# Performance work log

Measured on AMD Instinct MI355X. Metric: run time of the kernel, lower is better.

Reference implementation:

```python
import jax, jax.numpy as jnp
import numpy as np

OUT_FEATURES = 8192
IN_FEATURES = 4096  # d
CODEBOOK_SIZE = 16  # 2**bits, bits=4
BATCH = 32


def setup_inputs() -> dict:
    key = jax.random.key(0)
    k_x, k_idx, k_cb, k_r, k_b = jax.random.split(key, 5)
    x = jax.random.normal(k_x, (BATCH, IN_FEATURES), dtype=jnp.float32)
    indices = jax.random.randint(k_idx, (OUT_FEATURES, IN_FEATURES), 0, CODEBOOK_SIZE, dtype=jnp.int32)
    codebook = jax.random.normal(k_cb, (CODEBOOK_SIZE,), dtype=jnp.float32)
    # rotation matrix from the quantizer (orthogonal in the real impl; random here,
    # scaled for numerical stability)
    rotation_matrix = jax.random.normal(k_r, (IN_FEATURES, IN_FEATURES), dtype=jnp.float32) / np.sqrt(IN_FEATURES).astype(np.float32)
    bias = jax.random.normal(k_b, (OUT_FEATURES,), dtype=jnp.float32)
    return {"x": x, "indices": indices, "codebook": codebook,
            "rotation_matrix": rotation_matrix, "bias": bias}


def reference(x, indices, codebook, rotation_matrix, bias):
    # Dequantize: gather per-element codewords, then rotate back to weight space.
    # quantize was idx = Q(R @ w_row)  =>  w_row \approx R^T @ codebook[idx]
    codes = codebook[indices]                      # [O, D] gather
    weight = jnp.matmul(codes, rotation_matrix)    # [O, D]  (== (R^T @ c) per row)
    # F.linear(x, W, b) = x @ W^T + b
    return jnp.matmul(x, weight.T) + bias          # [B, O]
```

## Files before the change

kernel.cpp:

```cpp
#include <hip/hip_runtime.h>
#include <hip/hip_bf16.h>


#define IN_F 4096
#define OUT_F 8192
#define BATCH 32
#define TS 264

typedef short bf16x8s __attribute__((ext_vector_type(8)));
typedef float f32x4 __attribute__((ext_vector_type(4)));
typedef int   i32x4 __attribute__((ext_vector_type(4)));

__device__ __forceinline__ unsigned short f2bf(float f) {
    union { float f; unsigned int u; } v; v.f = f;
    unsigned int u = v.u;
    return (unsigned short)((u + 0x7fffu + ((u >> 16) & 1u)) >> 16);
}

__global__ void __launch_bounds__(256, 3) k1_xRT(const float* __restrict__ x,
                                                 const float* __restrict__ R,
                                                 const float* __restrict__ bias,
                                                 float* __restrict__ out,
                                                 float* __restrict__ y_ws) {
    __shared__ unsigned short Bl[64 * TS];
    __shared__ unsigned short Al[32 * TS];

    const int tid  = threadIdx.x;
    const int jt   = blockIdx.x & 63;
    const int kq   = blockIdx.x >> 6;
    const int j0   = jt * 64;
    const int k0   = kq * 256;
    const int wave = tid >> 6, lane = tid & 63;
    const int n = lane & 15, quad = lane >> 4;

    f32x4 rv[16];
    #pragma unroll
    for (int jj = 0; jj < 16; ++jj) {
        int f = tid + jj * 256;
        int row = f >> 6, c4 = f & 63;
        rv[jj] = __builtin_nontemporal_load(
            (const f32x4*)(R + (size_t)(j0 + row) * IN_F + k0 + c4 * 4));
    }
    f32x4 xv[8];
    #pragma unroll
    for (int ii = 0; ii < 8; ++ii) {
        int f = tid + ii * 256;
        int row = f >> 6, c4 = f & 63;
        xv[ii] = *(const f32x4*)(x + (size_t)row * IN_F + k0 + c4 * 4);
    }
    {
        int id = blockIdx.x * 256 + tid;
        out[id] = bias[id & (OUT_F - 1)];
    }

    #pragma unroll
    for (int jj = 0; jj < 16; ++jj) {
        int f = tid + jj * 256;
        int row = f >> 6, c4 = f & 63;
        ushort4 pv;
        pv.x = f2bf(rv[jj].x); pv.y = f2bf(rv[jj].y);
        pv.z = f2bf(rv[jj].z); pv.w = f2bf(rv[jj].w);
        *(ushort4*)&Bl[row * TS + c4 * 4] = pv;
    }
    #pragma unroll
    for (int ii = 0; ii < 8; ++ii) {
        int f = tid + ii * 256;
        int row = f >> 6, c4 = f & 63;
        ushort4 pv;
        pv.x = f2bf(xv[ii].x); pv.y = f2bf(xv[ii].y);
        pv.z = f2bf(xv[ii].z); pv.w = f2bf(xv[ii].w);
        *(ushort4*)&Al[row * TS + c4 * 4] = pv;
    }
    __syncthreads();

    f32x4 acc0 = {0.f, 0.f, 0.f, 0.f};
    f32x4 acc1 = {0.f, 0.f, 0.f, 0.f};
    #pragma unroll
    for (int ks = 0; ks < 8; ++ks) {
        bf16x8s bfr = *(const bf16x8s*)&Bl[(wave * 16 + n) * TS + ks * 32 + quad * 8];
        bf16x8s a0  = *(const bf16x8s*)&Al[n * TS + ks * 32 + quad * 8];
        bf16x8s a1  = *(const bf16x8s*)&Al[(16 + n) * TS + ks * 32 + quad * 8];
        acc0 = __builtin_amdgcn_mfma_f32_16x16x32_bf16(a0, bfr, acc0, 0, 0, 0);
        acc1 = __builtin_amdgcn_mfma_f32_16x16x32_bf16(a1, bfr, acc1, 0, 0, 0);
    }

    const int jcol = j0 + wave * 16 + n;
    #pragma unroll
    for (int r = 0; r < 4; ++r) {
        int br = quad * 4 + r;
        atomicAdd(&y_ws[(size_t)br * IN_F + jcol], acc0[r]);
        atomicAdd(&y_ws[(size_t)(br + 16) * IN_F + jcol], acc1[r]);
    }
}

__global__ void __launch_bounds__(256, 3) k2_out(const int* __restrict__ idx,
                                                 const float* __restrict__ cb,
                                                 const float* __restrict__ yws,
                                                 float* __restrict__ out) {
    __shared__ unsigned short Bl[64 * TS];
    __shared__ unsigned short Al[32 * TS];
    __shared__ unsigned int cbp[256];

    const int tid = threadIdx.x;
    const int ot = blockIdx.x & 127;
    const int kq = blockIdx.x >> 7;
    const int o0 = ot * 64;
    const int k0 = kq * 256;
    const int wave = tid >> 6, lane = tid & 63;
    const int n = lane & 15, quad = lane >> 4;

    i32x4 iv[16];
    #pragma unroll
    for (int jj = 0; jj < 16; ++jj) {
        int f = tid + jj * 256;
        int row = f >> 6, c4 = f & 63;
        iv[jj] = __builtin_nontemporal_load(
            (const i32x4*)(idx + (size_t)(o0 + row) * IN_F + k0 + c4 * 4));
    }
    f32x4 fv[8];
    #pragma unroll
    for (int ii = 0; ii < 8; ++ii) {
        int f = tid + ii * 256;
        int row = f >> 6, c4 = f & 63;
        fv[ii] = *(const f32x4*)(yws + (size_t)row * IN_F + k0 + c4 * 4);
    }

    {
        unsigned int lo = f2bf(cb[tid & 15]);
        unsigned int hi = f2bf(cb[tid >> 4]);
        cbp[tid] = lo | (hi << 16);
    }
    __syncthreads();

    #pragma unroll
    for (int jj = 0; jj < 16; ++jj) {
        int f = tid + jj * 256;
        int row = f >> 6, c4 = f & 63;
        unsigned int key0 = (unsigned int)iv[jj].x | ((unsigned int)iv[jj].y << 4);
        unsigned int key1 = (unsigned int)iv[jj].z | ((unsigned int)iv[jj].w << 4);
        uint2 pv;
        pv.x = cbp[key0];
        pv.y = cbp[key1];
        *(uint2*)&Bl[row * TS + c4 * 4] = pv;
    }
    #pragma unroll
    for (int ii = 0; ii < 8; ++ii) {
        int f = tid + ii * 256;
        int row = f >> 6, c4 = f & 63;
        ushort4 pv;
        pv.x = f2bf(fv[ii].x); pv.y = f2bf(fv[ii].y);
        pv.z = f2bf(fv[ii].z); pv.w = f2bf(fv[ii].w);
        *(ushort4*)&Al[row * TS + c4 * 4] = pv;
    }
    __syncthreads();

    f32x4 acc0 = {0.f, 0.f, 0.f, 0.f};
    f32x4 acc1 = {0.f, 0.f, 0.f, 0.f};
    #pragma unroll
    for (int ks = 0; ks < 8; ++ks) {
        bf16x8s bfr = *(const bf16x8s*)&Bl[(wave * 16 + n) * TS + ks * 32 + quad * 8];
        bf16x8s a0  = *(const bf16x8s*)&Al[n * TS + ks * 32 + quad * 8];
        bf16x8s a1  = *(const bf16x8s*)&Al[(16 + n) * TS + ks * 32 + quad * 8];
        acc0 = __builtin_amdgcn_mfma_f32_16x16x32_bf16(a0, bfr, acc0, 0, 0, 0);
        acc1 = __builtin_amdgcn_mfma_f32_16x16x32_bf16(a1, bfr, acc1, 0, 0, 0);
    }

    const int ocol = o0 + wave * 16 + n;
    #pragma unroll
    for (int r = 0; r < 4; ++r) {
        int br = quad * 4 + r;
        atomicAdd(&out[(size_t)br * OUT_F + ocol], acc0[r]);
        atomicAdd(&out[(size_t)(br + 16) * OUT_F + ocol], acc1[r]);
    }
}

extern "C" void kernel_launch(void* const* d_in, const int* in_sizes, int n_in,
                              void* d_out, int out_size, void* d_ws, size_t ws_size,
                              hipStream_t stream) {
    (void)in_sizes; (void)n_in; (void)out_size; (void)ws_size;
    const float* x       = (const float*)d_in[0];
    const int*   indices = (const int*)d_in[1];
    const float* cb      = (const float*)d_in[2];
    const float* R       = (const float*)d_in[3];
    const float* bias    = (const float*)d_in[4];
    float* out  = (float*)d_out;
    float* y_ws = (float*)d_ws;

    hipMemsetAsync(y_ws, 0, (size_t)BATCH * IN_F * sizeof(float), stream);
    k1_xRT<<<dim3(1024), dim3(256), 0, stream>>>(x, R, bias, out, y_ws);
    k2_out<<<dim3(2048), dim3(256), 0, stream>>>(indices, cb, y_ws, out);
}
```

Measured before the change: 240.6 us.

## Double-buffer LDS tiles and halve grid with 512-wide K per block

Each block now covers a 512-wide K range split into four 128-wide chunks. Loads of the next chunk are issued into registers while the current chunk is converted to bf16 and fed to MFMA, using two LDS buffers. This halves the number of blocks and therefore the atomicAdd traffic on the output and workspace, and overlaps global loads with compute. The cost is more syncs per block and fewer blocks to spread across CUs. The bias init is widened to float2 stores to match the smaller grid.

```diff
diff --git a/kernel.cpp b/kernel.cpp
--- a/kernel.cpp
+++ b/kernel.cpp
@@ -1,11 +1,10 @@
 #include <hip/hip_runtime.h>
-#include <hip/hip_bf16.h>
 
 
 #define IN_F 4096
 #define OUT_F 8192
 #define BATCH 32
-#define TS 264
+#define TSa 136
 
 typedef short bf16x8s __attribute__((ext_vector_type(8)));
 typedef float f32x4 __attribute__((ext_vector_type(4)));
@@ -15,6 +14,61 @@
     union { float f; unsigned int u; } v; v.f = f;
     unsigned int u = v.u;
     return (unsigned short)((u + 0x7fffu + ((u >> 16) & 1u)) >> 16);
+}
+
+__device__ __forceinline__ void load8_nt(f32x4* dst, const float* base, int coff) {
+    #pragma unroll
+    for (int jj = 0; jj < 8; ++jj)
+        dst[jj] = __builtin_nontemporal_load((const f32x4*)(base + (size_t)jj * 8 * IN_F + coff));
+}
+__device__ __forceinline__ void load8i_nt(i32x4* dst, const int* base, int coff) {
+    #pragma unroll
+    for (int jj = 0; jj < 8; ++jj)
+        dst[jj] = __builtin_nontemporal_load((const i32x4*)(base + (size_t)jj * 8 * IN_F + coff));
+}
+__device__ __forceinline__ void load4(f32x4* dst, const float* base, int coff) {
+    #pragma unroll
+    for (int ii = 0; ii < 4; ++ii)
+        dst[ii] = *(const f32x4*)(base + (size_t)ii * 8 * IN_F + coff);
+}
+__device__ __forceinline__ void cvt8(unsigned short* lds, int lb, const f32x4* v) {
+    #pragma unroll
+    for (int jj = 0; jj < 8; ++jj) {
+        ushort4 pv;
+        pv.x = f2bf(v[jj].x); pv.y = f2bf(v[jj].y);
+        pv.z = f2bf(v[jj].z); pv.w = f2bf(v[jj].w);
+        *(ushort4*)&lds[lb + jj * 8 * TSa] = pv;
+    }
+}
+__device__ __forceinline__ void cvt4(unsigned short* lds, int lb, const f32x4* v) {
+    #pragma unroll
+    for (int ii = 0; ii < 4; ++ii) {
+        ushort4 pv;
+        pv.x = f2bf(v[ii].x); pv.y = f2bf(v[ii].y);
+        pv.z = f2bf(v[ii].z); pv.w = f2bf(v[ii].w);
+        *(ushort4*)&lds[lb + ii * 8 * TSa] = pv;
+    }
+}
+__device__ __forceinline__ void cvt_codes(unsigned short* lds, int lb, const i32x4* v,
+                                          const unsigned int* cbp) {
+    #pragma unroll
+    for (int jj = 0; jj < 8; ++jj) {
+        unsigned int key0 = (unsigned int)v[jj].x | ((unsigned int)v[jj].y << 4);
+        unsigned int key1 = (unsigned int)v[jj].z | ((unsigned int)v[jj].w << 4);
+        uint2 pv; pv.x = cbp[key0]; pv.y = cbp[key1];
+        *(uint2*)&lds[lb + jj * 8 * TSa] = pv;
+    }
+}
+__device__ __forceinline__ void mmstep(const unsigned short* B, const unsigned short* A,
+                                       int bo, int ao, f32x4& acc0, f32x4& acc1) {
+    #pragma unroll
+    for (int ks = 0; ks < 4; ++ks) {
+        bf16x8s bfr = *(const bf16x8s*)&B[bo + ks * 32];
+        bf16x8s a0  = *(const bf16x8s*)&A[ao + ks * 32];
+        bf16x8s a1  = *(const bf16x8s*)&A[ao + 16 * TSa + ks * 32];
+        acc0 = __builtin_amdgcn_mfma_f32_16x16x32_bf16(a0, bfr, acc0, 0, 0, 0);
+        acc1 = __builtin_amdgcn_mfma_f32_16x16x32_bf16(a1, bfr, acc1, 0, 0, 0);
+    }
 }
 
 __global__ void __launch_bounds__(256, 3) k1_xRT(const float* __restrict__ x,
@@ -22,67 +76,57 @@
                                                  const float* __restrict__ bias,
                                                  float* __restrict__ out,
                                                  float* __restrict__ y_ws) {
-    __shared__ unsigned short Bl[64 * TS];
-    __shared__ unsigned short Al[32 * TS];
+    __shared__ unsigned short Bl[2][64 * TSa];
+    __shared__ unsigned short Al[2][32 * TSa];
 
     const int tid  = threadIdx.x;
     const int jt   = blockIdx.x & 63;
     const int kq   = blockIdx.x >> 6;
     const int j0   = jt * 64;
-    const int k0   = kq * 256;
+    const int kb   = kq * 512;
     const int wave = tid >> 6, lane = tid & 63;
     const int n = lane & 15, quad = lane >> 4;
-
-    f32x4 rv[16];
-    #pragma unroll
-    for (int jj = 0; jj < 16; ++jj) {
-        int f = tid + jj * 256;
-        int row = f >> 6, c4 = f & 63;
-        rv[jj] = __builtin_nontemporal_load(
-            (const f32x4*)(R + (size_t)(j0 + row) * IN_F + k0 + c4 * 4));
-    }
-    f32x4 xv[8];
-    #pragma unroll
-    for (int ii = 0; ii < 8; ++ii) {
-        int f = tid + ii * 256;
-        int row = f >> 6, c4 = f & 63;
-        xv[ii] = *(const f32x4*)(x + (size_t)row * IN_F + k0 + c4 * 4);
-    }
+    const int r0 = tid >> 5, c4 = tid & 31;
+
+    const float* rbase = R + (size_t)(j0 + r0) * IN_F + kb + c4 * 4;
+    const float* xbase = x + (size_t)r0 * IN_F + kb + c4 * 4;
+    const int lb = r0 * TSa + c4 * 4;
+    const int bo = (wave * 16 + n) * TSa + quad * 8;
+    const int ao = n * TSa + quad * 8;
+
+    f32x4 rvA[8], rvB[8], xvA[4], xvB[4];
+    load8_nt(rvA, rbase, 0);
+    load4(xvA, xbase, 0);
+
     {
-        int id = blockIdx.x * 256 + tid;
-        out[id] = bias[id & (OUT_F - 1)];
-    }
-
-    #pragma unroll
-    for (int jj = 0; jj < 16; ++jj) {
-        int f = tid + jj * 256;
-        int row = f >> 6, c4 = f & 63;
-        ushort4 pv;
-        pv.x = f2bf(rv[jj].x); pv.y = f2bf(rv[jj].y);
-        pv.z = f2bf(rv[jj].z); pv.w = f2bf(rv[jj].w);
-        *(ushort4*)&Bl[row * TS + c4 * 4] = pv;
-    }
-    #pragma unroll
-    for (int ii = 0; ii < 8; ++ii) {
-        int f = tid + ii * 256;
-        int row = f >> 6, c4 = f & 63;
-        ushort4 pv;
-        pv.x = f2bf(xv[ii].x); pv.y = f2bf(xv[ii].y);
-        pv.z = f2bf(xv[ii].z); pv.w = f2bf(xv[ii].w);
-        *(ushort4*)&Al[row * TS + c4 * 4] = pv;
-    }
-    __syncthreads();
+        int e = (blockIdx.x * 256 + tid) * 2;
+        float2 bv;
+        bv.x = bias[e & (OUT_F - 1)];
+        bv.y = bias[(e + 1) & (OUT_F - 1)];
+        *(float2*)(out + e) = bv;
+    }
 
     f32x4 acc0 = {0.f, 0.f, 0.f, 0.f};
     f32x4 acc1 = {0.f, 0.f, 0.f, 0.f};
-    #pragma unroll
-    for (int ks = 0; ks < 8; ++ks) {
-        bf16x8s bfr = *(const bf16x8s*)&Bl[(wave * 16 + n) * TS + ks * 32 + quad * 8];
-        bf16x8s a0  = *(const bf16x8s*)&Al[n * TS + ks * 32 + quad * 8];
-        bf16x8s a1  = *(const bf16x8s*)&Al[(16 + n) * TS + ks * 32 + quad * 8];
-        acc0 = __builtin_amdgcn_mfma_f32_16x16x32_bf16(a0, bfr, acc0, 0, 0, 0);
-        acc1 = __builtin_amdgcn_mfma_f32_16x16x32_bf16(a1, bfr, acc1, 0, 0, 0);
-    }
+
+    load8_nt(rvB, rbase, 128); load4(xvB, xbase, 128);
+    cvt8(Bl[0], lb, rvA); cvt4(Al[0], lb, xvA);
+    __syncthreads();
+    mmstep(Bl[0], Al[0], bo, ao, acc0, acc1);
+
+    load8_nt(rvA, rbase, 256); load4(xvA, xbase, 256);
+    cvt8(Bl[1], lb, rvB); cvt4(Al[1], lb, xvB);
+    __syncthreads();
+    mmstep(Bl[1], Al[1], bo, ao, acc0, acc1);
+
+    load8_nt(rvB, rbase, 384); load4(xvB, xbase, 384);
+    cvt8(Bl[0], lb, rvA); cvt4(Al[0], lb, xvA);
+    __syncthreads();
+    mmstep(Bl[0], Al[0], bo, ao, acc0, acc1);
+
+    cvt8(Bl[1], lb, rvB); cvt4(Al[1], lb, xvB);
+    __syncthreads();
+    mmstep(Bl[1], Al[1], bo, ao, acc0, acc1);
 
     const int jcol = j0 + wave * 16 + n;
     #pragma unroll
@@ -97,73 +141,57 @@
                                                  const float* __restrict__ cb,
                                                  const float* __restrict__ yws,
                                                  float* __restrict__ out) {
-    __shared__ unsigned short Bl[64 * TS];
-    __shared__ unsigned short Al[32 * TS];
+    __shared__ unsigned short Bl[2][64 * TSa];
+    __shared__ unsigned short Al[2][32 * TSa];
     __shared__ unsigned int cbp[256];
 
     const int tid = threadIdx.x;
     const int ot = blockIdx.x & 127;
     const int kq = blockIdx.x >> 7;
     const int o0 = ot * 64;
-    const int k0 = kq * 256;
+    const int kb = kq * 512;
     const int wave = tid >> 6, lane = tid & 63;
     const int n = lane & 15, quad = lane >> 4;
-
-    i32x4 iv[16];
-    #pragma unroll
-    for (int jj = 0; jj < 16; ++jj) {
-        int f = tid + jj * 256;
-        int row = f >> 6, c4 = f & 63;
-        iv[jj] = __builtin_nontemporal_load(
-            (const i32x4*)(idx + (size_t)(o0 + row) * IN_F + k0 + c4 * 4));
-    }
-    f32x4 fv[8];
-    #pragma unroll
-    for (int ii = 0; ii < 8; ++ii) {
-        int f = tid + ii * 256;
-        int row = f >> 6, c4 = f & 63;
-        fv[ii] = *(const f32x4*)(yws + (size_t)row * IN_F + k0 + c4 * 4);
-    }
-
+    const int r0 = tid >> 5, c4 = tid & 31;
+
+    const int*   ibase = idx + (size_t)(o0 + r0) * IN_F + kb + c4 * 4;
+    const float* ybase = yws + (size_t)r0 * IN_F + kb + c4 * 4;
+    const int lb = r0 * TSa + c4 * 4;
+    const int bo = (wave * 16 + n) * TSa + quad * 8;
+    const int ao = n * TSa + quad * 8;
+
+    i32x4 ivA[8], ivB[8];
+    f32x4 fvA[4], fvB[4];
+    load8i_nt(ivA, ibase, 0);
+    load4(fvA, ybase, 0);
     {
         unsigned int lo = f2bf(cb[tid & 15]);
         unsigned int hi = f2bf(cb[tid >> 4]);
         cbp[tid] = lo | (hi << 16);
     }
-    __syncthreads();
-
-    #pragma unroll
-    for (int jj = 0; jj < 16; ++jj) {
-        int f = tid + jj * 256;
-        int row = f >> 6, c4 = f & 63;
-        unsigned int key0 = (unsigned int)iv[jj].x | ((unsigned int)iv[jj].y << 4);
-        unsigned int key1 = (unsigned int)iv[jj].z | ((unsigned int)iv[jj].w << 4);
-        uint2 pv;
-        pv.x = cbp[key0];
-        pv.y = cbp[key1];
-        *(uint2*)&Bl[row * TS + c4 * 4] = pv;
-    }
-    #pragma unroll
-    for (int ii = 0; ii < 8; ++ii) {
-        int f = tid + ii * 256;
-        int row = f >> 6, c4 = f & 63;
-        ushort4 pv;
-        pv.x = f2bf(fv[ii].x); pv.y = f2bf(fv[ii].y);
-        pv.z = f2bf(fv[ii].z); pv.w = f2bf(fv[ii].w);
-        *(ushort4*)&Al[row * TS + c4 * 4] = pv;
-    }
+    load8i_nt(ivB, ibase, 128); load4(fvB, ybase, 128);
     __syncthreads();
 
     f32x4 acc0 = {0.f, 0.f, 0.f, 0.f};
     f32x4 acc1 = {0.f, 0.f, 0.f, 0.f};
-    #pragma unroll
-    for (int ks = 0; ks < 8; ++ks) {
-        bf16x8s bfr = *(const bf16x8s*)&Bl[(wave * 16 + n) * TS + ks * 32 + quad * 8];
-        bf16x8s a0  = *(const bf16x8s*)&Al[n * TS + ks * 32 + quad * 8];
-        bf16x8s a1  = *(const bf16x8s*)&Al[(16 + n) * TS + ks * 32 + quad * 8];
-        acc0 = __builtin_amdgcn_mfma_f32_16x16x32_bf16(a0, bfr, acc0, 0, 0, 0);
-        acc1 = __builtin_amdgcn_mfma_f32_16x16x32_bf16(a1, bfr, acc1, 0, 0, 0);
-    }
+
+    cvt_codes(Bl[0], lb, ivA, cbp); cvt4(Al[0], lb, fvA);
+    __syncthreads();
+    mmstep(Bl[0], Al[0], bo, ao, acc0, acc1);
+
+    load8i_nt(ivA, ibase, 256); load4(fvA, ybase, 256);
+    cvt_codes(Bl[1], lb, ivB, cbp); cvt4(Al[1], lb, fvB);
+    __syncthreads();
+    mmstep(Bl[1], Al[1], bo, ao, acc0, acc1);
+
+    load8i_nt(ivB, ibase, 384); load4(fvB, ybase, 384);
+    cvt_codes(Bl[0], lb, ivA, cbp); cvt4(Al[0], lb, fvA);
+    __syncthreads();
+    mmstep(Bl[0], Al[0], bo, ao, acc0, acc1);
+
+    cvt_codes(Bl[1], lb, ivB, cbp); cvt4(Al[1], lb, fvB);
+    __syncthreads();
+    mmstep(Bl[1], Al[1], bo, ao, acc0, acc1);
 
     const int ocol = o0 + wave * 16 + n;
     #pragma unroll
@@ -187,6 +215,6 @@
     float* y_ws = (float*)d_ws;
 
     hipMemsetAsync(y_ws, 0, (size_t)BATCH * IN_F * sizeof(float), stream);
-    k1_xRT<<<dim3(1024), dim3(256), 0, stream>>>(x, R, bias, out, y_ws);
-    k2_out<<<dim3(2048), dim3(256), 0, stream>>>(indices, cb, y_ws, out);
-}
+    k1_xRT<<<dim3(512),  dim3(256), 0, stream>>>(x, R, bias, out, y_ws);
+    k2_out<<<dim3(1024), dim3(256), 0, stream>>>(indices, cb, y_ws, out);
+}
```

Measured after the change: 235.0 us. -2.4%, faster.
